# Optimization experiments

Measured on AMD Instinct MI355X. Metric: run time of the kernel, lower is better.

Reference implementation:

```python
import jax, jax.numpy as jnp
import numpy as np

N = 100_000
E = 1_600_000
IN_FT, HID, OUT = 512, 128, 64


def setup_inputs() -> dict:
    key = jax.random.key(0)
    ks = jax.random.split(key, 7)
    x = jax.random.normal(ks[0], (N, IN_FT), dtype=jnp.float32)
    edge_index = jax.random.randint(ks[1], (2, E), 0, N, dtype=jnp.int32)
    edge_weight = jax.random.uniform(ks[2], (E,), dtype=jnp.float32)
    W1 = jax.random.normal(ks[3], (IN_FT, HID), dtype=jnp.float32) * 0.05
    b1 = jnp.zeros((HID,), dtype=jnp.float32)
    W2 = jax.random.normal(ks[4], (HID, OUT), dtype=jnp.float32) * 0.05
    b2 = jnp.zeros((OUT,), dtype=jnp.float32)
    return {"x": x, "edge_index": edge_index, "edge_weight": edge_weight,
            "W1": W1, "b1": b1, "W2": W2, "b2": b2}


def reference(x, edge_index, edge_weight, W1, b1, W2, b2):
    n = x.shape[0]
    row, col = edge_index[0], edge_index[1]
    # PyG gcn_norm: add self-loops with weight 1, symmetric normalization
    loop = jnp.arange(n, dtype=row.dtype)
    r = jnp.concatenate([row, loop])
    c = jnp.concatenate([col, loop])
    w = jnp.concatenate([edge_weight, jnp.ones((n,), edge_weight.dtype)])
    deg = jax.ops.segment_sum(w, c, num_segments=n)
    dinv = jnp.where(deg > 0, jax.lax.rsqrt(deg), 0.0)
    norm = dinv[r] * w * dinv[c]  # [E + N]

    def conv(h, W, b):
        h = h @ W                                  # [N, F_out]
        msg = norm[:, None] * h[r]                 # gather source nodes
        return jax.ops.segment_sum(msg, c, num_segments=n) + b

    h = jax.nn.relu(conv(x, W1, b1))
    # dropout: inference mode (training=False) -> identity
    out = conv(h, W2, b2)
    return jax.nn.log_softmax(out, axis=1)
```

## Files before the change

### kernel.cpp

```cpp
#include <hip/hip_runtime.h>
#include <hip/hip_fp16.h>


constexpr int NN  = 100000;
constexpr int NE  = 1600000;
constexpr int FIN = 512;
constexpr int FH  = 128;
constexpr int FO  = 64;
constexpr int CAP = 64;

constexpr int NBLK1 = 512;
constexpr int EPB   = NE / NBLK1;
constexpr int NBKT  = 196;
constexpr int BCAP  = 9728;
constexpr int NWT   = FIN * FH + FH * FO;
constexpr int NG    = (NN + 127) / 128;

constexpr float WSCALE  = 32767.0f;
constexpr float IWSCALE = 1.0f / 32767.0f;

typedef _Float16 f16x8 __attribute__((ext_vector_type(8)));
typedef float    f32x4 __attribute__((ext_vector_type(4)));

union F16Frag { _Float16 f[8]; short4 s[2]; f16x8 v; };

__device__ __forceinline__ void gload16(const void* g, void* l) {
    __builtin_amdgcn_global_load_lds(
        (const __attribute__((address_space(1))) void*)g,
        (__attribute__((address_space(3))) void*)l,
        16, 0, 0);
}


__global__ __launch_bounds__(256) void k_prep(const float* __restrict__ W1,
                                              const float* __restrict__ W2,
                                              int* __restrict__ bcur,
                                              _Float16* __restrict__ w1t,
                                              _Float16* __restrict__ w2t) {
    int i = blockIdx.x * 256 + threadIdx.x;
    if (i < NBKT) bcur[i] = 0;
    if (i < FIN * FH) {
        int k = i >> 7, c = i & 127;
        w1t[c * FIN + k] = (_Float16)W1[i];
    } else if (i < NWT) {
        int j = i - FIN * FH;
        int k = j >> 6, c = j & 63;
        w2t[c * FH + k] = (_Float16)W2[j];
    }
}


union MegaShared {
    struct {
        float    Asf[128 * 64];
        _Float16 Bs[128 * 64];
    } g;
    struct {
        unsigned long long buf[EPB];
        int hist[NBKT];
        int curs[NBKT];
    } b;
};

__global__ __launch_bounds__(256) void k_mega(const float* __restrict__ X,
                                              const _Float16* __restrict__ w1t,
                                              _Float16* __restrict__ H1,
                                              const int* __restrict__ rowi,
                                              const int* __restrict__ coli,
                                              const float* __restrict__ ew,
                                              int* __restrict__ bcur,
                                              unsigned long long* __restrict__ binned) {
    __shared__ MegaShared sm;
    const int tid = threadIdx.x;

    if (blockIdx.x >= NG) {
        const int bb   = blockIdx.x - NG;
        const int base = bb * EPB;
        for (int i = tid; i < NBKT; i += 256) sm.b.hist[i] = 0;
        __syncthreads();
        for (int i = tid; i < EPB; i += 256) {
            int e = base + i;
            int c = coli[e];
            unsigned wq = __float2uint_rn(ew[e] * WSCALE);
            sm.b.buf[i] = ((unsigned long long)(unsigned)c << 32)
                        | (unsigned long long)((wq << 17) | (unsigned)rowi[e]);
            atomicAdd(&sm.b.hist[c >> 9], 1);
        }
        __syncthreads();
        if (tid < NBKT) sm.b.curs[tid] = atomicAdd(&bcur[tid], sm.b.hist[tid]);
        __syncthreads();
        for (int i = tid; i < EPB; i += 256) {
            unsigned long long v = sm.b.buf[i];
            int b = (int)(v >> 41);
            int pos = atomicAdd(&sm.b.curs[b], 1);
            if ((unsigned)pos < BCAP) binned[(size_t)b * BCAP + pos] = v;
        }
        return;
    }

    const int wid = tid >> 6, l = tid & 63;
    const int wr = wid >> 1, wc = wid & 1;
    const int l15 = l & 15, lg = l >> 4;
    const int brow = blockIdx.x * 128;

    f32x4 acc[4][4];
#pragma unroll
    for (int m = 0; m < 4; ++m)
#pragma unroll
        for (int n = 0; n < 4; ++n) acc[m][n] = (f32x4){0.f, 0.f, 0.f, 0.f};

    const int rA = wid * 32 + (l >> 4);
    const int sA = l & 15;
    const int rB = wid * 32 + (l >> 3);
    const int sB = l & 7;

    for (int k0 = 0; k0 < FIN; k0 += 64) {
#pragma unroll
        for (int j = 0; j < 8; ++j) {
            int r  = rA + j * 4;
            int sg = sA ^ (r & 15);
            gload16(&X[(size_t)min(brow + r, NN - 1) * FIN + k0 + sg * 4],
                    &sm.g.Asf[wid * 2048 + j * 256]);
        }
#pragma unroll
        for (int j = 0; j < 4; ++j) {
            int r  = rB + j * 8;
            int sg = sB ^ (r & 7);
            gload16(&w1t[(size_t)r * FIN + k0 + sg * 8],
                    &sm.g.Bs[wid * 2048 + j * 512]);
        }
        __syncthreads();
#pragma unroll
        for (int ks = 0; ks < 2; ++ks) {
            F16Frag au[4], bu[4];
#pragma unroll
            for (int m = 0; m < 4; ++m) {
                int row = wr * 64 + m * 16 + l15;
                int slo = ks * 8 + lg;
                float4 lo = *(const float4*)&sm.g.Asf[row * 64 + ((slo       ^ (row & 15)) * 4)];
                float4 hi = *(const float4*)&sm.g.Asf[row * 64 + (((slo + 4) ^ (row & 15)) * 4)];
                au[m].f[0] = (_Float16)lo.x; au[m].f[1] = (_Float16)lo.y;
                au[m].f[2] = (_Float16)lo.z; au[m].f[3] = (_Float16)lo.w;
                au[m].f[4] = (_Float16)hi.x; au[m].f[5] = (_Float16)hi.y;
                au[m].f[6] = (_Float16)hi.z; au[m].f[7] = (_Float16)hi.w;
            }
#pragma unroll
            for (int n = 0; n < 4; ++n) {
                int row = wc * 64 + n * 16 + l15;
                int sb  = ks * 4 + (lg >> 1);
                int wi  = (lg & 1) * 4;
                bu[n].s[0] = *(const short4*)&sm.g.Bs[row * 64 + ((sb       ^ (row & 7)) * 8) + wi];
                bu[n].s[1] = *(const short4*)&sm.g.Bs[row * 64 + (((sb + 2) ^ (row & 7)) * 8) + wi];
            }
#pragma unroll
            for (int m = 0; m < 4; ++m)
#pragma unroll
                for (int n = 0; n < 4; ++n)
                    acc[m][n] = __builtin_amdgcn_mfma_f32_16x16x32_f16(
                        au[m].v, bu[n].v, acc[m][n], 0, 0, 0);
        }
        __syncthreads();
    }
#pragma unroll
    for (int m = 0; m < 4; ++m)
#pragma unroll
        for (int n = 0; n < 4; ++n) {
            int gcol = wc * 64 + n * 16 + l15;
#pragma unroll
            for (int r4 = 0; r4 < 4; ++r4) {
                int gr = brow + wr * 64 + m * 16 + lg * 4 + r4;
                if (gr < NN) H1[(size_t)gr * FH + gcol] = (_Float16)acc[m][n][r4];
            }
        }
}


__global__ __launch_bounds__(256) void k_pass2(const int* __restrict__ bcur,
                                               const unsigned long long* __restrict__ binned,
                                               unsigned* __restrict__ pay,
                                               int* __restrict__ cursor,
                                               float* __restrict__ dinv) {
    __shared__ int   cnt[512];
    __shared__ float wsum[512];
    const int t = threadIdx.x, b = blockIdx.x;
    for (int i = t; i < 512; i += 256) { cnt[i] = 0; wsum[i] = 0.f; }
    __syncthreads();
    const int total = min(bcur[b], BCAP);
    const int nbase = b * 512;
    for (int i = t; i < total; i += 256) {
        unsigned long long v = binned[(size_t)b * BCAP + i];
        int c9 = (int)((v >> 32) & 511);
        unsigned lo = (unsigned)v;
        int pos = atomicAdd(&cnt[c9], 1);
        atomicAdd(&wsum[c9], (float)(lo >> 17) * IWSCALE);
        if (pos < CAP) pay[(size_t)(nbase + c9) * CAP + pos] = lo;
    }
    __syncthreads();
    for (int i = t; i < 512; i += 256) {
        int node = nbase + i;
        if (node < NN) {
            cursor[node] = cnt[i];
            dinv[node]   = rsqrtf(1.0f + wsum[i]);
        }
    }
}


__global__ __launch_bounds__(256) void k_gemm2(const _Float16* __restrict__ H2,
                                               const _Float16* __restrict__ w2t,
                                               _Float16* __restrict__ H3) {
    __shared__ __align__(16) _Float16 As[64 * 128];
    __shared__ __align__(16) _Float16 Bs[64 * 128];
    const int tid  = threadIdx.x;
    const int brow = blockIdx.x * 64;
    const int wid = tid >> 6, l = tid & 63;
    const int wr = wid >> 1, wc = wid & 1;
    const int l15 = l & 15, lg = l >> 4;

    f32x4 acc[2][2];
#pragma unroll
    for (int m = 0; m < 2; ++m)
#pragma unroll
        for (int n = 0; n < 2; ++n) acc[m][n] = (f32x4){0.f, 0.f, 0.f, 0.f};

    {
        int ar = tid >> 2, part = tid & 3, grow = brow + ar;
#pragma unroll
        for (int j = 0; j < 4; ++j) {
            int slot = part * 4 + j;
            int4 v = make_int4(0, 0, 0, 0);
            if (grow < NN) v = *(const int4*)&H2[(size_t)grow * FH + slot * 8];
            *(int4*)&As[ar * 128 + ((slot ^ (ar & 15)) * 8)] = v;
            *(int4*)&Bs[ar * 128 + ((slot ^ (ar & 15)) * 8)] =
                *(const int4*)&w2t[ar * FH + slot * 8];
        }
    }
    __syncthreads();
#pragma unroll
    for (int ks = 0; ks < 4; ++ks) {
        F16Frag au[2], bu[2];
        int klo = ks * 32 + 4 * lg;
        int khi = klo + 16;
#pragma unroll
        for (int m = 0; m < 2; ++m) {
            int row = wr * 32 + m * 16 + l15;
            int sw  = row & 15;
            au[m].s[0] = *(const short4*)&As[row * 128 + (((klo >> 3) ^ sw) * 8) + (klo & 7)];
            au[m].s[1] = *(const short4*)&As[row * 128 + (((khi >> 3) ^ sw) * 8) + (khi & 7)];
        }
#pragma unroll
        for (int n = 0; n < 2; ++n) {
            int row = wc * 32 + n * 16 + l15;
            int sw  = row & 15;
            bu[n].s[0] = *(const short4*)&Bs[row * 128 + (((klo >> 3) ^ sw) * 8) + (klo & 7)];
            bu[n].s[1] = *(const short4*)&Bs[row * 128 + (((khi >> 3) ^ sw) * 8) + (khi & 7)];
        }
#pragma unroll
        for (int m = 0; m < 2; ++m)
#pragma unroll
            for (int n = 0; n < 2; ++n)
                acc[m][n] = __builtin_amdgcn_mfma_f32_16x16x32_f16(
                    au[m].v, bu[n].v, acc[m][n], 0, 0, 0);
    }
#pragma unroll
    for (int m = 0; m < 2; ++m)
#pragma unroll
        for (int n = 0; n < 2; ++n) {
            int gcol = wc * 32 + n * 16 + l15;
#pragma unroll
            for (int r4 = 0; r4 < 4; ++r4) {
                int gr = brow + wr * 32 + m * 16 + lg * 4 + r4;
                if (gr < NN) H3[(size_t)gr * FO + gcol] = (_Float16)acc[m][n][r4];
            }
        }
}


__global__ __launch_bounds__(256) void k_agg1(const int* __restrict__ cursor,
                                              const unsigned* __restrict__ pay,
                                              const float* __restrict__ dinv,
                                              const __half* __restrict__ H1,
                                              const float* __restrict__ b1,
                                              __half* __restrict__ H2) {
    int node = (blockIdx.x * 256 + threadIdx.x) >> 6;
    int lane = threadIdx.x & 63;
    if (node >= NN) return;
    const int f = lane * 2;
    float dc  = dinv[node];
    float dcs = dc * IWSCALE;
    float2 hc = __half22float2(*(const __half2*)&H1[(size_t)node * FH + f]);
    float a0x = dc * dc * hc.x, a0y = dc * dc * hc.y;
    float a1x = 0, a1y = 0, a2x = 0, a2y = 0, a3x = 0, a3y = 0;
    int cnt = min(max(cursor[node], 0), CAP);
    const unsigned* p = &pay[(size_t)node * CAP];
    int e = 0;
    for (; e + 8 <= cnt; e += 8) {
        uint4 pa = *(const uint4*)&p[e];
        uint4 pb = *(const uint4*)&p[e + 4];
        int s0 = pa.x & 0x1FFFF, s1 = pa.y & 0x1FFFF, s2 = pa.z & 0x1FFFF, s3 = pa.w & 0x1FFFF;
        int s4 = pb.x & 0x1FFFF, s5 = pb.y & 0x1FFFF, s6 = pb.z & 0x1FFFF, s7 = pb.w & 0x1FFFF;
        float w0 = (float)(pa.x >> 17) * dcs * dinv[s0];
        float w1 = (float)(pa.y >> 17) * dcs * dinv[s1];
        float w2 = (float)(pa.z >> 17) * dcs * dinv[s2];
        float w3 = (float)(pa.w >> 17) * dcs * dinv[s3];
        float w4 = (float)(pb.x >> 17) * dcs * dinv[s4];
        float w5 = (float)(pb.y >> 17) * dcs * dinv[s5];
        float w6 = (float)(pb.z >> 17) * dcs * dinv[s6];
        float w7 = (float)(pb.w >> 17) * dcs * dinv[s7];
        float2 g0 = __half22float2(*(const __half2*)&H1[(size_t)s0 * FH + f]);
        float2 g1 = __half22float2(*(const __half2*)&H1[(size_t)s1 * FH + f]);
        float2 g2 = __half22float2(*(const __half2*)&H1[(size_t)s2 * FH + f]);
        float2 g3 = __half22float2(*(const __half2*)&H1[(size_t)s3 * FH + f]);
        float2 g4 = __half22float2(*(const __half2*)&H1[(size_t)s4 * FH + f]);
        float2 g5 = __half22float2(*(const __half2*)&H1[(size_t)s5 * FH + f]);
        float2 g6 = __half22float2(*(const __half2*)&H1[(size_t)s6 * FH + f]);
        float2 g7 = __half22float2(*(const __half2*)&H1[(size_t)s7 * FH + f]);
        a0x += w0 * g0.x; a0y += w0 * g0.y;  a1x += w1 * g1.x; a1y += w1 * g1.y;
        a2x += w2 * g2.x; a2y += w2 * g2.y;  a3x += w3 * g3.x; a3y += w3 * g3.y;
        a0x += w4 * g4.x; a0y += w4 * g4.y;  a1x += w5 * g5.x; a1y += w5 * g5.y;
        a2x += w6 * g6.x; a2y += w6 * g6.y;  a3x += w7 * g7.x; a3y += w7 * g7.y;
    }
    for (; e < cnt; ++e) {
        unsigned v = p[e];
        int s = v & 0x1FFFF;
        float w = (float)(v >> 17) * dcs * dinv[s];
        float2 g = __half22float2(*(const __half2*)&H1[(size_t)s * FH + f]);
        a0x += w * g.x; a0y += w * g.y;
    }
    float vx = a0x + a1x + a2x + a3x + b1[f];
    float vy = a0y + a1y + a2y + a3y + b1[f + 1];
    vx = vx > 0.f ? vx : 0.f;
    vy = vy > 0.f ? vy : 0.f;
    *(__half2*)&H2[(size_t)node * FH + f] = __floats2half2_rn(vx, vy);
}


__global__ __launch_bounds__(256) void k_agg2(const int* __restrict__ cursor,
                                              const unsigned* __restrict__ pay,
                                              const float* __restrict__ dinv,
                                              const __half* __restrict__ H3,
                                              const float* __restrict__ b2,
                                              float* __restrict__ out) {
    int node = (blockIdx.x * 256 + threadIdx.x) >> 6;
    int lane = threadIdx.x & 63;
    if (node >= NN) return;
    float dc  = dinv[node];
    float dcs = dc * IWSCALE;
    float a0 = dc * dc * __half2float(H3[(size_t)node * FO + lane]);
    float a1 = 0, a2 = 0, a3 = 0;
    int cnt = min(max(cursor[node], 0), CAP);
    const unsigned* p = &pay[(size_t)node * CAP];
    int e = 0;
    for (; e + 8 <= cnt; e += 8) {
        uint4 pa = *(const uint4*)&p[e];
        uint4 pb = *(const uint4*)&p[e + 4];
        int s0 = pa.x & 0x1FFFF, s1 = pa.y & 0x1FFFF, s2 = pa.z & 0x1FFFF, s3 = pa.w & 0x1FFFF;
        int s4 = pb.x & 0x1FFFF, s5 = pb.y & 0x1FFFF, s6 = pb.z & 0x1FFFF, s7 = pb.w & 0x1FFFF;
        float w0 = (float)(pa.x >> 17) * dcs * dinv[s0];
        float w1 = (float)(pa.y >> 17) * dcs * dinv[s1];
        float w2 = (float)(pa.z >> 17) * dcs * dinv[s2];
        float w3 = (float)(pa.w >> 17) * dcs * dinv[s3];
        float w4 = (float)(pb.x >> 17) * dcs * dinv[s4];
        float w5 = (float)(pb.y >> 17) * dcs * dinv[s5];
        float w6 = (float)(pb.z >> 17) * dcs * dinv[s6];
        float w7 = (float)(pb.w >> 17) * dcs * dinv[s7];
        a0 += w0 * __half2float(H3[(size_t)s0 * FO + lane]);
        a1 += w1 * __half2float(H3[(size_t)s1 * FO + lane]);
        a2 += w2 * __half2float(H3[(size_t)s2 * FO + lane]);
        a3 += w3 * __half2float(H3[(size_t)s3 * FO + lane]);
        a0 += w4 * __half2float(H3[(size_t)s4 * FO + lane]);
        a1 += w5 * __half2float(H3[(size_t)s5 * FO + lane]);
        a2 += w6 * __half2float(H3[(size_t)s6 * FO + lane]);
        a3 += w7 * __half2float(H3[(size_t)s7 * FO + lane]);
    }
    for (; e < cnt; ++e) {
        unsigned v = p[e];
        int s = v & 0x1FFFF;
        float w = (float)(v >> 17) * dcs * dinv[s];
        a0 += w * __half2float(H3[(size_t)s * FO + lane]);
    }
    float v = a0 + a1 + a2 + a3 + b2[lane];
    float m = v;
#pragma unroll
    for (int s = 32; s; s >>= 1) m = fmaxf(m, __shfl_xor(m, s));
    float ex = expf(v - m);
    float sum = ex;
#pragma unroll
    for (int s = 32; s; s >>= 1) sum += __shfl_xor(sum, s);
    out[(size_t)node * FO + lane] = v - m - logf(sum);
}


extern "C" void kernel_launch(void* const* d_in, const int* in_sizes, int n_in,
                              void* d_out, int out_size, void* d_ws, size_t ws_size,
                              hipStream_t stream) {
    const float* x   = (const float*)d_in[0];
    const int*   ei  = (const int*)d_in[1];
    const int*   row = ei;
    const int*   col = ei + NE;
    const float* ew  = (const float*)d_in[2];
    const float* W1  = (const float*)d_in[3];
    const float* b1  = (const float*)d_in[4];
    const float* W2  = (const float*)d_in[5];
    const float* b2  = (const float*)d_in[6];
    float* out = (float*)d_out;

    int*       bcur   = (int*)d_ws;
    int*       cursor = bcur + 256;
    float*     dinv   = (float*)(cursor + 102400);
    _Float16*  w1t    = (_Float16*)(dinv + 102400);
    _Float16*  w2t    = w1t + FIN * FH;
    unsigned long long* binned = (unsigned long long*)(w2t + FH * FO);
    unsigned*  pay    = (unsigned*)(binned + (size_t)NBKT * BCAP);
    _Float16*  H1     = (_Float16*)(pay + (size_t)NN * CAP);
    _Float16*  H2     = H1 + (size_t)NN * FH;
    _Float16*  H3     = H2 + (size_t)NN * FH;

    k_prep <<<(NWT + 255) / 256, 256, 0, stream>>>(W1, W2, bcur, w1t, w2t);
    k_mega <<<NG + NBLK1, 256, 0, stream>>>(x, w1t, H1, row, col, ew, bcur, binned);
    k_pass2<<<NBKT, 256, 0, stream>>>(bcur, binned, pay, cursor, dinv);

    k_agg1 <<<(NN * 64 + 255) / 256, 256, 0, stream>>>(cursor, pay, dinv,
                                                       (const __half*)H1, b1, (__half*)H2);
    k_gemm2<<<(NN + 63) / 64, 256, 0, stream>>>(H2, w2t, H3);
    k_agg2 <<<(NN * 64 + 255) / 256, 256, 0, stream>>>(cursor, pay, dinv,
                                                       (const __half*)H3, b2, out);
}
```

Measured before the change: 251.6 us.

## Fuse layer-1 aggregation with second GEMM via shared-memory tile

Merges the first aggregation and the H2·W2 GEMM into one kernel. Each block aggregates 16 nodes (4 per wavefront) into a swizzled LDS tile, then runs MFMA against W2 read straight from global memory. This removes the H2 round trip through global memory and one kernel launch. In exchange, each wavefront now handles 4 nodes serially, which lowers latency hiding in the gather phase. W2 fragments are also re-read from global/L2 by every block.

```diff
diff --git a/kernel.cpp b/kernel.cpp
--- a/kernel.cpp
+++ b/kernel.cpp
@@ -206,132 +206,94 @@
 }
 
 
-__global__ __launch_bounds__(256) void k_gemm2(const _Float16* __restrict__ H2,
+__global__ __launch_bounds__(256) void k_agg1g(const int* __restrict__ cursor,
+                                               const unsigned* __restrict__ pay,
+                                               const float* __restrict__ dinv,
+                                               const __half* __restrict__ H1,
+                                               const float* __restrict__ b1,
                                                const _Float16* __restrict__ w2t,
                                                _Float16* __restrict__ H3) {
-    __shared__ __align__(16) _Float16 As[64 * 128];
-    __shared__ __align__(16) _Float16 Bs[64 * 128];
-    const int tid  = threadIdx.x;
-    const int brow = blockIdx.x * 64;
+    __shared__ __align__(16) _Float16 hr[16 * 128];
+    const int tid = threadIdx.x;
     const int wid = tid >> 6, l = tid & 63;
-    const int wr = wid >> 1, wc = wid & 1;
     const int l15 = l & 15, lg = l >> 4;
-
-    f32x4 acc[2][2];
-#pragma unroll
-    for (int m = 0; m < 2; ++m)
-#pragma unroll
-        for (int n = 0; n < 2; ++n) acc[m][n] = (f32x4){0.f, 0.f, 0.f, 0.f};
-
-    {
-        int ar = tid >> 2, part = tid & 3, grow = brow + ar;
-#pragma unroll
-        for (int j = 0; j < 4; ++j) {
-            int slot = part * 4 + j;
-            int4 v = make_int4(0, 0, 0, 0);
-            if (grow < NN) v = *(const int4*)&H2[(size_t)grow * FH + slot * 8];
-            *(int4*)&As[ar * 128 + ((slot ^ (ar & 15)) * 8)] = v;
-            *(int4*)&Bs[ar * 128 + ((slot ^ (ar & 15)) * 8)] =
-                *(const int4*)&w2t[ar * FH + slot * 8];
-        }
+    const int nb = blockIdx.x * 16;
+
+    for (int i = 0; i < 4; ++i) {
+        const int r    = wid * 4 + i;
+        const int node = nb + r;
+        const int f    = l * 2;
+        float vx = 0.f, vy = 0.f;
+        if (node < NN) {
+            float dc  = dinv[node];
+            float dcs = dc * IWSCALE;
+            float2 hc = __half22float2(*(const __half2*)&H1[(size_t)node * FH + f]);
+            float a0x = dc * dc * hc.x, a0y = dc * dc * hc.y;
+            float a1x = 0, a1y = 0, a2x = 0, a2y = 0, a3x = 0, a3y = 0;
+            int cnt = min(max(cursor[node], 0), CAP);
+            const unsigned* p = &pay[(size_t)node * CAP];
+            int e = 0;
+            for (; e + 8 <= cnt; e += 8) {
+                uint4 pa = *(const uint4*)&p[e];
+                uint4 pb = *(const uint4*)&p[e + 4];
+                int s0 = pa.x & 0x1FFFF, s1 = pa.y & 0x1FFFF, s2 = pa.z & 0x1FFFF, s3 = pa.w & 0x1FFFF;
+                int s4 = pb.x & 0x1FFFF, s5 = pb.y & 0x1FFFF, s6 = pb.z & 0x1FFFF, s7 = pb.w & 0x1FFFF;
+                float w0 = (float)(pa.x >> 17) * dcs * dinv[s0];
+                float w1 = (float)(pa.y >> 17) * dcs * dinv[s1];
+                float w2 = (float)(pa.z >> 17) * dcs * dinv[s2];
+                float w3 = (float)(pa.w >> 17) * dcs * dinv[s3];
+                float w4 = (float)(pb.x >> 17) * dcs * dinv[s4];
+                float w5 = (float)(pb.y >> 17) * dcs * dinv[s5];
+                float w6 = (float)(pb.z >> 17) * dcs * dinv[s6];
+                float w7 = (float)(pb.w >> 17) * dcs * dinv[s7];
+                float2 g0 = __half22float2(*(const __half2*)&H1[(size_t)s0 * FH + f]);
+                float2 g1 = __half22float2(*(const __half2*)&H1[(size_t)s1 * FH + f]);
+                float2 g2 = __half22float2(*(const __half2*)&H1[(size_t)s2 * FH + f]);
+                float2 g3 = __half22float2(*(const __half2*)&H1[(size_t)s3 * FH + f]);
+                float2 g4 = __half22float2(*(const __half2*)&H1[(size_t)s4 * FH + f]);
+                float2 g5 = __half22float2(*(const __half2*)&H1[(size_t)s5 * FH + f]);
+                float2 g6 = __half22float2(*(const __half2*)&H1[(size_t)s6 * FH + f]);
+                float2 g7 = __half22float2(*(const __half2*)&H1[(size_t)s7 * FH + f]);
+                a0x += w0 * g0.x; a0y += w0 * g0.y;  a1x += w1 * g1.x; a1y += w1 * g1.y;
+                a2x += w2 * g2.x; a2y += w2 * g2.y;  a3x += w3 * g3.x; a3y += w3 * g3.y;
+                a0x += w4 * g4.x; a0y += w4 * g4.y;  a1x += w5 * g5.x; a1y += w5 * g5.y;
+                a2x += w6 * g6.x; a2y += w6 * g6.y;  a3x += w7 * g7.x; a3y += w7 * g7.y;
+            }
+            for (; e < cnt; ++e) {
+                unsigned v = p[e];
+                int s = v & 0x1FFFF;
+                float w = (float)(v >> 17) * dcs * dinv[s];
+                float2 g = __half22float2(*(const __half2*)&H1[(size_t)s * FH + f]);
+                a0x += w * g.x; a0y += w * g.y;
+            }
+            vx = a0x + a1x + a2x + a3x + b1[f];
+            vy = a0y + a1y + a2y + a3y + b1[f + 1];
+            vx = vx > 0.f ? vx : 0.f;
+            vy = vy > 0.f ? vy : 0.f;
+        }
+        int slot = f >> 3, wi = f & 7;
+        __half2 hv = __floats2half2_rn(vx, vy);
+        *(__half2*)&hr[r * 128 + ((slot ^ (r & 15)) * 8) + wi] = hv;
     }
     __syncthreads();
+    f32x4 acc = (f32x4){0.f, 0.f, 0.f, 0.f};
+    const _Float16* pb = &w2t[(size_t)(wid * 16 + l15) * FH];
 #pragma unroll
     for (int ks = 0; ks < 4; ++ks) {
-        F16Frag au[2], bu[2];
         int klo = ks * 32 + 4 * lg;
         int khi = klo + 16;
-#pragma unroll
-        for (int m = 0; m < 2; ++m) {
-            int row = wr * 32 + m * 16 + l15;
-            int sw  = row & 15;
-            au[m].s[0] = *(const short4*)&As[row * 128 + (((klo >> 3) ^ sw) * 8) + (klo & 7)];
-            au[m].s[1] = *(const short4*)&As[row * 128 + (((khi >> 3) ^ sw) * 8) + (khi & 7)];
-        }
-#pragma unroll
-        for (int n = 0; n < 2; ++n) {
-            int row = wc * 32 + n * 16 + l15;
-            int sw  = row & 15;
-            bu[n].s[0] = *(const short4*)&Bs[row * 128 + (((klo >> 3) ^ sw) * 8) + (klo & 7)];
-            bu[n].s[1] = *(const short4*)&Bs[row * 128 + (((khi >> 3) ^ sw) * 8) + (khi & 7)];
-        }
-#pragma unroll
-        for (int m = 0; m < 2; ++m)
-#pragma unroll
-            for (int n = 0; n < 2; ++n)
-                acc[m][n] = __builtin_amdgcn_mfma_f32_16x16x32_f16(
-                    au[m].v, bu[n].v, acc[m][n], 0, 0, 0);
-    }
-#pragma unroll
-    for (int m = 0; m < 2; ++m)
-#pragma unroll
-        for (int n = 0; n < 2; ++n) {
-            int gcol = wc * 32 + n * 16 + l15;
-#pragma unroll
-            for (int r4 = 0; r4 < 4; ++r4) {
-                int gr = brow + wr * 32 + m * 16 + lg * 4 + r4;
-                if (gr < NN) H3[(size_t)gr * FO + gcol] = (_Float16)acc[m][n][r4];
-            }
-        }
-}
-
-
-__global__ __launch_bounds__(256) void k_agg1(const int* __restrict__ cursor,
-                                              const unsigned* __restrict__ pay,
-                                              const float* __restrict__ dinv,
-                                              const __half* __restrict__ H1,
-                                              const float* __restrict__ b1,
-                                              __half* __restrict__ H2) {
-    int node = (blockIdx.x * 256 + threadIdx.x) >> 6;
-    int lane = threadIdx.x & 63;
-    if (node >= NN) return;
-    const int f = lane * 2;
-    float dc  = dinv[node];
-    float dcs = dc * IWSCALE;
-    float2 hc = __half22float2(*(const __half2*)&H1[(size_t)node * FH + f]);
-    float a0x = dc * dc * hc.x, a0y = dc * dc * hc.y;
-    float a1x = 0, a1y = 0, a2x = 0, a2y = 0, a3x = 0, a3y = 0;
-    int cnt = min(max(cursor[node], 0), CAP);
-    const unsigned* p = &pay[(size_t)node * CAP];
-    int e = 0;
-    for (; e + 8 <= cnt; e += 8) {
-        uint4 pa = *(const uint4*)&p[e];
-        uint4 pb = *(const uint4*)&p[e + 4];
-        int s0 = pa.x & 0x1FFFF, s1 = pa.y & 0x1FFFF, s2 = pa.z & 0x1FFFF, s3 = pa.w & 0x1FFFF;
-        int s4 = pb.x & 0x1FFFF, s5 = pb.y & 0x1FFFF, s6 = pb.z & 0x1FFFF, s7 = pb.w & 0x1FFFF;
-        float w0 = (float)(pa.x >> 17) * dcs * dinv[s0];
-        float w1 = (float)(pa.y >> 17) * dcs * dinv[s1];
-        float w2 = (float)(pa.z >> 17) * dcs * dinv[s2];
-        float w3 = (float)(pa.w >> 17) * dcs * dinv[s3];
-        float w4 = (float)(pb.x >> 17) * dcs * dinv[s4];
-        float w5 = (float)(pb.y >> 17) * dcs * dinv[s5];
-        float w6 = (float)(pb.z >> 17) * dcs * dinv[s6];
-        float w7 = (float)(pb.w >> 17) * dcs * dinv[s7];
-        float2 g0 = __half22float2(*(const __half2*)&H1[(size_t)s0 * FH + f]);
-        float2 g1 = __half22float2(*(const __half2*)&H1[(size_t)s1 * FH + f]);
-        float2 g2 = __half22float2(*(const __half2*)&H1[(size_t)s2 * FH + f]);
-        float2 g3 = __half22float2(*(const __half2*)&H1[(size_t)s3 * FH + f]);
-        float2 g4 = __half22float2(*(const __half2*)&H1[(size_t)s4 * FH + f]);
-        float2 g5 = __half22float2(*(const __half2*)&H1[(size_t)s5 * FH + f]);
-        float2 g6 = __half22float2(*(const __half2*)&H1[(size_t)s6 * FH + f]);
-        float2 g7 = __half22float2(*(const __half2*)&H1[(size_t)s7 * FH + f]);
-        a0x += w0 * g0.x; a0y += w0 * g0.y;  a1x += w1 * g1.x; a1y += w1 * g1.y;
-        a2x += w2 * g2.x; a2y += w2 * g2.y;  a3x += w3 * g3.x; a3y += w3 * g3.y;
-        a0x += w4 * g4.x; a0y += w4 * g4.y;  a1x += w5 * g5.x; a1y += w5 * g5.y;
-        a2x += w6 * g6.x; a2y += w6 * g6.y;  a3x += w7 * g7.x; a3y += w7 * g7.y;
-    }
-    for (; e < cnt; ++e) {
-        unsigned v = p[e];
-        int s = v & 0x1FFFF;
-        float w = (float)(v >> 17) * dcs * dinv[s];
-        float2 g = __half22float2(*(const __half2*)&H1[(size_t)s * FH + f]);
-        a0x += w * g.x; a0y += w * g.y;
-    }
-    float vx = a0x + a1x + a2x + a3x + b1[f];
-    float vy = a0y + a1y + a2y + a3y + b1[f + 1];
-    vx = vx > 0.f ? vx : 0.f;
-    vy = vy > 0.f ? vy : 0.f;
-    *(__half2*)&H2[(size_t)node * FH + f] = __floats2half2_rn(vx, vy);
+        F16Frag au, bu;
+        au.s[0] = *(const short4*)&hr[l15 * 128 + (((klo >> 3) ^ l15) * 8) + (klo & 7)];
+        au.s[1] = *(const short4*)&hr[l15 * 128 + (((khi >> 3) ^ l15) * 8) + (khi & 7)];
+        bu.s[0] = *(const short4*)&pb[klo];
+        bu.s[1] = *(const short4*)&pb[khi];
+        acc = __builtin_amdgcn_mfma_f32_16x16x32_f16(au.v, bu.v, acc, 0, 0, 0);
+    }
+#pragma unroll
+    for (int r4 = 0; r4 < 4; ++r4) {
+        int gr = nb + lg * 4 + r4;
+        if (gr < NN) H3[(size_t)gr * FO + wid * 16 + l15] = (_Float16)acc[r4];
+    }
 }
 
 
@@ -413,16 +375,14 @@
     unsigned long long* binned = (unsigned long long*)(w2t + FH * FO);
     unsigned*  pay    = (unsigned*)(binned + (size_t)NBKT * BCAP);
     _Float16*  H1     = (_Float16*)(pay + (size_t)NN * CAP);
-    _Float16*  H2     = H1 + (size_t)NN * FH;
-    _Float16*  H3     = H2 + (size_t)NN * FH;
+    _Float16*  H3     = H1 + (size_t)NN * FH;
 
     k_prep <<<(NWT + 255) / 256, 256, 0, stream>>>(W1, W2, bcur, w1t, w2t);
     k_mega <<<NG + NBLK1, 256, 0, stream>>>(x, w1t, H1, row, col, ew, bcur, binned);
     k_pass2<<<NBKT, 256, 0, stream>>>(bcur, binned, pay, cursor, dinv);
 
-    k_agg1 <<<(NN * 64 + 255) / 256, 256, 0, stream>>>(cursor, pay, dinv,
-                                                       (const __half*)H1, b1, (__half*)H2);
-    k_gemm2<<<(NN + 63) / 64, 256, 0, stream>>>(H2, w2t, H3);
+    k_agg1g<<<(NN + 15) / 16, 256, 0, stream>>>(cursor, pay, dinv,
+                                                (const __half*)H1, b1, w2t, H3);
     k_agg2 <<<(NN * 64 + 255) / 256, 256, 0, stream>>>(cursor, pay, dinv,
                                                        (const __half*)H3, b2, out);
 }
```

Result: slower. 261.7 us (+4.0%).
